# Kernel optimization log

Measured on AMD Instinct MI355X. Metric: run time of the kernel, lower is better.

## Reference

```python
import jax, jax.numpy as jnp
import numpy as np

N_USERS = 100000
N_ITEMS = 50000
N_NODES = N_USERS + N_ITEMS
N_EDGES = 3000000
EMBED_DIM = 64
N_LAYERS = 3


def setup_inputs() -> dict:
    key = jax.random.key(0)
    k1, k2, k3, k4, k5 = jax.random.split(key, 5)
    user_emb = 0.1 * jax.random.normal(k1, (N_USERS, EMBED_DIM), dtype=jnp.float32)
    item_emb = 0.1 * jax.random.normal(k2, (N_ITEMS, EMBED_DIM), dtype=jnp.float32)
    adj_rows = jax.random.randint(k3, (N_EDGES,), 0, N_NODES, dtype=jnp.int32)
    adj_cols = jax.random.randint(k4, (N_EDGES,), 0, N_NODES, dtype=jnp.int32)
    # mimic symmetric normalization scale (~1/avg_degree) so repeated SpMM stays stable
    avg_degree = N_EDGES / N_NODES
    adj_vals = jax.random.uniform(k5, (N_EDGES,), dtype=jnp.float32) / jnp.float32(avg_degree)
    return {"user_emb": user_emb, "item_emb": item_emb,
            "adj_rows": adj_rows, "adj_cols": adj_cols, "adj_vals": adj_vals}


def _spmm(rows, cols, vals, x):
    # y[r] = sum_{e: rows[e]==r} vals[e] * x[cols[e]]   (COO SpMM)
    msgs = vals[:, None] * x[cols]          # [E, d] gathered messages
    return jax.ops.segment_sum(msgs, rows, num_segments=N_NODES)


def reference(user_emb, item_emb, adj_rows, adj_cols, adj_vals):
    all_emb = jnp.concatenate([user_emb, item_emb], axis=0)  # [N, d]
    acc = all_emb
    cur = all_emb
    for _ in range(N_LAYERS):
        cur = _spmm(adj_rows, adj_cols, adj_vals, cur)
        acc = acc + cur
    final_emb = acc / jnp.float32(N_LAYERS + 1)  # mean over stacked layers
    return final_emb[:N_USERS], final_emb[N_USERS:]
```

## Files before the change

kernel.cpp:

```cpp
#include <hip/hip_runtime.h>
#include <cstddef>
#include <cstdint>

#define N_USERS 100000
#define N_ITEMS 50000
#define N_NODES 150000
#define N_EDGES 3000000

#define NBKT 586
#define BCHUNK 8192
#define ABLK ((N_EDGES + BCHUNK - 1) / BCHUNK)
#define NCLS 16
#define SCHUNK 3
#define PADMAX (256 * 7)

#define VMAX  0.05f
#define QSCALE (16384.0f / VMAX)
#define DEQ    (VMAX / 16384.0f)

typedef unsigned int uint32;
typedef unsigned short ushort16;

__device__ __forceinline__ ushort16 f2b(float f) {
    uint32 b = __float_as_uint(f);
    b += 0x7FFFu + ((b >> 16) & 1u);
    return (ushort16)(b >> 16);
}
__device__ __forceinline__ float b2f(ushort16 h) {
    return __uint_as_float(((uint32)h) << 16);
}

#define CVT_BLOCKS ((N_NODES * 16 + 255) / 256)

__global__ __launch_bounds__(256) void k_cvt_count(const float* __restrict__ user,
                                                   const float* __restrict__ item,
                                                   ushort16* __restrict__ allb,
                                                   const int* __restrict__ rows,
                                                   int* __restrict__ bucket_cnt) {
    if (blockIdx.x < CVT_BLOCKS) {
        int i = blockIdx.x * blockDim.x + threadIdx.x;
        const int total4 = N_NODES * 16;
        if (i >= total4) return;
        const int user4 = N_USERS * 16;
        float4 v = (i < user4) ? ((const float4*)user)[i]
                               : ((const float4*)item)[i - user4];
        ushort4 h;
        h.x = f2b(v.x); h.y = f2b(v.y); h.z = f2b(v.z); h.w = f2b(v.w);
        ((ushort4*)allb)[i] = h;
        return;
    }
    __shared__ int hist[NBKT];
    int t = threadIdx.x;
    for (int j = t; j < NBKT; j += 256) hist[j] = 0;
    __syncthreads();
    int blk = blockIdx.x - CVT_BLOCKS;
    int s0 = blk * BCHUNK;
    int e0 = min(s0 + BCHUNK, N_EDGES);
    for (int i = s0 + t * 4; i < e0; i += 1024) {
        int4 r4 = *(const int4*)(rows + i);
        atomicAdd(&hist[r4.x >> 8], 1); atomicAdd(&hist[r4.y >> 8], 1);
        atomicAdd(&hist[r4.z >> 8], 1); atomicAdd(&hist[r4.w >> 8], 1);
    }
    __syncthreads();
    for (int j = t; j < NBKT; j += 256)
        if (hist[j]) atomicAdd(&bucket_cnt[j], hist[j]);
}

__global__ __launch_bounds__(1024) void k_bucket_scan(const int* __restrict__ bucket_cnt,
                                                      int* __restrict__ bucket_start,
                                                      int* __restrict__ bucket_cursor) {
    __shared__ int sh[1024];
    int t = threadIdx.x;
    sh[t] = (t < NBKT) ? bucket_cnt[t] : 0;
    __syncthreads();
    for (int off = 1; off < 1024; off <<= 1) {
        int add = (t >= off) ? sh[t - off] : 0;
        __syncthreads();
        sh[t] += add;
        __syncthreads();
    }
    if (t < NBKT) {
        int st = (t == 0) ? 0 : sh[t - 1];
        bucket_start[t] = st;
        bucket_cursor[t] = st;
    }
    if (t == 0) bucket_start[NBKT] = N_EDGES;
}

__global__ __launch_bounds__(256) void k_bucket_scatter(const int* __restrict__ rows,
                                                        const int* __restrict__ cols,
                                                        const float* __restrict__ vals,
                                                        int* __restrict__ bucket_cursor,
                                                        int2* __restrict__ ebuf) {
    __shared__ int  hist[NBKT];
    __shared__ int  lstart[NBKT];
    __shared__ int  curs[NBKT];
    __shared__ int  gbase[NBKT];
    __shared__ int  psum[256];
    __shared__ int2 stage[BCHUNK];
    int t = threadIdx.x;
    for (int j = t; j < NBKT; j += 256) hist[j] = 0;
    __syncthreads();
    int s0 = blockIdx.x * BCHUNK;
    int e0 = min(s0 + BCHUNK, N_EDGES);
    int n = e0 - s0;
    for (int i = s0 + t * 4; i < e0; i += 1024) {
        int4 r4 = *(const int4*)(rows + i);
        atomicAdd(&hist[r4.x >> 8], 1); atomicAdd(&hist[r4.y >> 8], 1);
        atomicAdd(&hist[r4.z >> 8], 1); atomicAdd(&hist[r4.w >> 8], 1);
    }
    __syncthreads();
    int base = t * SCHUNK;
    int v0 = (base < NBKT) ? hist[base] : 0;
    int v1 = (base + 1 < NBKT) ? hist[base + 1] : 0;
    int v2 = (base + 2 < NBKT) ? hist[base + 2] : 0;
    psum[t] = v0 + v1 + v2;
    __syncthreads();
    for (int off = 1; off < 256; off <<= 1) {
        int add = (t >= off) ? psum[t - off] : 0;
        __syncthreads();
        psum[t] += add;
        __syncthreads();
    }
    int run = (t == 0) ? 0 : psum[t - 1];
    if (base < NBKT) {
        lstart[base] = run; curs[base] = run;
        if (v0) gbase[base] = atomicAdd(&bucket_cursor[base], v0);
        run += v0;
    }
    if (base + 1 < NBKT) {
        lstart[base + 1] = run; curs[base + 1] = run;
        if (v1) gbase[base + 1] = atomicAdd(&bucket_cursor[base + 1], v1);
        run += v1;
    }
    if (base + 2 < NBKT) {
        lstart[base + 2] = run; curs[base + 2] = run;
        if (v2) gbase[base + 2] = atomicAdd(&bucket_cursor[base + 2], v2);
        run += v2;
    }
    __syncthreads();
    for (int i = s0 + t * 4; i < e0; i += 1024) {
        int4   r4 = *(const int4*)(rows + i);
        int4   c4 = *(const int4*)(cols + i);
        float4 w4 = *(const float4*)(vals + i);
        int rr, cc, b, pos; float ww;
        rr = r4.x; cc = c4.x; ww = w4.x; b = rr >> 8;
        pos = atomicAdd(&curs[b], 1);
        stage[pos] = make_int2(cc | ((rr & 255) << 18), __float_as_int(ww));
        rr = r4.y; cc = c4.y; ww = w4.y; b = rr >> 8;
        pos = atomicAdd(&curs[b], 1);
        stage[pos] = make_int2(cc | ((rr & 255) << 18), __float_as_int(ww));
        rr = r4.z; cc = c4.z; ww = w4.z; b = rr >> 8;
        pos = atomicAdd(&curs[b], 1);
        stage[pos] = make_int2(cc | ((rr & 255) << 18), __float_as_int(ww));
        rr = r4.w; cc = c4.w; ww = w4.w; b = rr >> 8;
        pos = atomicAdd(&curs[b], 1);
        stage[pos] = make_int2(cc | ((rr & 255) << 18), __float_as_int(ww));
    }
    __syncthreads();
    for (int i = t; i < n; i += 256) {
        int2 ed = stage[i];
        int lo = 0, hi = NBKT - 1;
        while (lo < hi) {
            int mid = (lo + hi + 1) >> 1;
            if (lstart[mid] <= i) lo = mid; else hi = mid - 1;
        }
        int dst = gbase[lo] + (i - lstart[lo]);
        long long q; __builtin_memcpy(&q, &ed, 8);
        __builtin_nontemporal_store(q, (long long*)(ebuf + dst));
    }
}

__global__ __launch_bounds__(256) void k_csr_build(const int2* __restrict__ ebuf,
                                                   const int* __restrict__ bucket_start,
                                                   int* __restrict__ row_start,
                                                   int* __restrict__ row_end,
                                                   uint32* __restrict__ ecsr) {
    __shared__ int cnt2[256 * NCLS];
    __shared__ int psum[256];
    int b = blockIdx.x, t = threadIdx.x;
    int rbase = b << 8;
    for (int j = t; j < 256 * NCLS; j += 256) cnt2[j] = 0;
    __syncthreads();
    int s = bucket_start[b], e = bucket_start[b + 1];
    int wbase = s + b * PADMAX;
    for (int i = s + t; i < e; i += 256) {
        int2 ed = ebuf[i];
        int col = ed.x & 0x3FFFF;
        int key = (((ed.x >> 18) & 255) << 4) | (col >> 14);
        atomicAdd(&cnt2[key], 1);
    }
    __syncthreads();
    int base = t * NCLS;
    int vals[NCLS];
    int cnt_row = 0;
    #pragma unroll
    for (int j = 0; j < NCLS; ++j) { vals[j] = cnt2[base + j]; cnt_row += vals[j]; }
    int pcnt = (cnt_row + 7) & ~7;
    psum[t] = pcnt;
    __syncthreads();
    for (int off = 1; off < 256; off <<= 1) {
        int add = (t >= off) ? psum[t - off] : 0;
        __syncthreads();
        psum[t] += add;
        __syncthreads();
    }
    int run = psum[t] - pcnt;
    int rr = rbase + t;
    if (rr < N_NODES) {
        row_start[rr] = wbase + run;
        row_end[rr]   = wbase + run + pcnt;
    }
    int rl = run;
    #pragma unroll
    for (int j = 0; j < NCLS; ++j) { int c = vals[j]; cnt2[base + j] = rl; rl += c; }
    __syncthreads();
    for (int i = s + t; i < e; i += 256) {
        int2 ed = ebuf[i];
        int col = ed.x & 0x3FFFF;
        int key = (((ed.x >> 18) & 255) << 4) | (col >> 14);
        int pos = atomicAdd(&cnt2[key], 1);
        float w = __int_as_float(ed.y);
        int q = (int)(w * QSCALE + 0.5f);
        q = min(q, 16383);
        ecsr[wbase + pos] = (uint32)col | ((uint32)q << 18);
    }
    for (int j = cnt_row; j < pcnt; ++j) ecsr[wbase + run + j] = 0;
}

template <int LAYER>
__global__ __launch_bounds__(256) void k_spmm(const int* __restrict__ row_start,
                                              const int* __restrict__ row_end,
                                              const uint32* __restrict__ ecsr,
                                              const ushort16* __restrict__ x,
                                              ushort16* __restrict__ yb,
                                              const ushort16* __restrict__ e0b,
                                              const ushort16* __restrict__ y1b,
                                              float* __restrict__ out) {
    int gid = blockIdx.x * blockDim.x + threadIdx.x;
    int r = gid >> 6;
    int lane = threadIdx.x & 63;
    if (r >= N_NODES) return;
    int s = __builtin_amdgcn_readfirstlane(row_start[r]);
    int e = __builtin_amdgcn_readfirstlane(row_end[r]);
    float acc = 0.f;
    if (e > s) {
        uint32 c0 = __builtin_nontemporal_load(ecsr + s);
        uint32 c1 = __builtin_nontemporal_load(ecsr + s + 1);
        uint32 c2 = __builtin_nontemporal_load(ecsr + s + 2);
        uint32 c3 = __builtin_nontemporal_load(ecsr + s + 3);
        uint32 c4 = __builtin_nontemporal_load(ecsr + s + 4);
        uint32 c5 = __builtin_nontemporal_load(ecsr + s + 5);
        uint32 c6 = __builtin_nontemporal_load(ecsr + s + 6);
        uint32 c7 = __builtin_nontemporal_load(ecsr + s + 7);
        for (int i = s + 8; i < e; i += 8) {
            uint32 n0 = __builtin_nontemporal_load(ecsr + i);
            uint32 n1 = __builtin_nontemporal_load(ecsr + i + 1);
            uint32 n2 = __builtin_nontemporal_load(ecsr + i + 2);
            uint32 n3 = __builtin_nontemporal_load(ecsr + i + 3);
            uint32 n4 = __builtin_nontemporal_load(ecsr + i + 4);
            uint32 n5 = __builtin_nontemporal_load(ecsr + i + 5);
            uint32 n6 = __builtin_nontemporal_load(ecsr + i + 6);
            uint32 n7 = __builtin_nontemporal_load(ecsr + i + 7);
            acc += (float)(c0 >> 18) * b2f(x[(size_t)(c0 & 0x3FFFF) * 64 + lane]);
            acc += (float)(c1 >> 18) * b2f(x[(size_t)(c1 & 0x3FFFF) * 64 + lane]);
            acc += (float)(c2 >> 18) * b2f(x[(size_t)(c2 & 0x3FFFF) * 64 + lane]);
            acc += (float)(c3 >> 18) * b2f(x[(size_t)(c3 & 0x3FFFF) * 64 + lane]);
            acc += (float)(c4 >> 18) * b2f(x[(size_t)(c4 & 0x3FFFF) * 64 + lane]);
            acc += (float)(c5 >> 18) * b2f(x[(size_t)(c5 & 0x3FFFF) * 64 + lane]);
            acc += (float)(c6 >> 18) * b2f(x[(size_t)(c6 & 0x3FFFF) * 64 + lane]);
            acc += (float)(c7 >> 18) * b2f(x[(size_t)(c7 & 0x3FFFF) * 64 + lane]);
            c0 = n0; c1 = n1; c2 = n2; c3 = n3;
            c4 = n4; c5 = n5; c6 = n6; c7 = n7;
        }
        acc += (float)(c0 >> 18) * b2f(x[(size_t)(c0 & 0x3FFFF) * 64 + lane]);
        acc += (float)(c1 >> 18) * b2f(x[(size_t)(c1 & 0x3FFFF) * 64 + lane]);
        acc += (float)(c2 >> 18) * b2f(x[(size_t)(c2 & 0x3FFFF) * 64 + lane]);
        acc += (float)(c3 >> 18) * b2f(x[(size_t)(c3 & 0x3FFFF) * 64 + lane]);
        acc += (float)(c4 >> 18) * b2f(x[(size_t)(c4 & 0x3FFFF) * 64 + lane]);
        acc += (float)(c5 >> 18) * b2f(x[(size_t)(c5 & 0x3FFFF) * 64 + lane]);
        acc += (float)(c6 >> 18) * b2f(x[(size_t)(c6 & 0x3FFFF) * 64 + lane]);
        acc += (float)(c7 >> 18) * b2f(x[(size_t)(c7 & 0x3FFFF) * 64 + lane]);
        acc *= DEQ;
    }

    size_t o = (size_t)r * 64 + lane;
    if constexpr (LAYER == 3) {
        ushort16 h0 = __builtin_nontemporal_load((const unsigned short*)e0b + o);
        ushort16 h1 = __builtin_nontemporal_load((const unsigned short*)y1b + o);
        ushort16 h2 = __builtin_nontemporal_load((const unsigned short*)x + o);
        __builtin_nontemporal_store(0.25f * (b2f(h0) + b2f(h1) + b2f(h2) + acc), out + o);
    } else {
        __builtin_nontemporal_store(f2b(acc), (unsigned short*)yb + o);
    }
}

__global__ __launch_bounds__(256) void k_init(const float* __restrict__ user,
                                              const float* __restrict__ item,
                                              float* __restrict__ cur,
                                              float* __restrict__ out) {
    int i = blockIdx.x * blockDim.x + threadIdx.x;
    const int total4 = N_NODES * 16;
    if (i >= total4) return;
    const int user4 = N_USERS * 16;
    float4 v = (i < user4) ? ((const float4*)user)[i]
                           : ((const float4*)item)[i - user4];
    ((float4*)cur)[i] = v;
    ((float4*)out)[i] = make_float4(0.25f * v.x, 0.25f * v.y,
                                    0.25f * v.z, 0.25f * v.w);
}

__global__ __launch_bounds__(256) void k_edge_atomic(const int* __restrict__ rows,
                                                     const int* __restrict__ cols,
                                                     const float* __restrict__ vals,
                                                     const float* __restrict__ x,
                                                     float* __restrict__ y) {
    long long gid = (long long)blockIdx.x * blockDim.x + threadIdx.x;
    int e = (int)(gid >> 6);
    int lane = threadIdx.x & 63;
    if (e >= N_EDGES) return;
    int r = rows[e], c = cols[e];
    float v = vals[e];
    atomicAdd(&y[r * 64 + lane], v * x[c * 64 + lane]);
}

__global__ __launch_bounds__(256) void k_accum(const float* __restrict__ y,
                                               float* __restrict__ out) {
    int i = blockIdx.x * blockDim.x + threadIdx.x;
    const int total4 = N_NODES * 16;
    if (i >= total4) return;
    float4 a = ((const float4*)y)[i];
    float4 o = ((float4*)out)[i];
    o.x += 0.25f * a.x; o.y += 0.25f * a.y;
    o.z += 0.25f * a.z; o.w += 0.25f * a.w;
    ((float4*)out)[i] = o;
}

extern "C" void kernel_launch(void* const* d_in, const int* in_sizes, int n_in,
                              void* d_out, int out_size, void* d_ws, size_t ws_size,
                              hipStream_t stream) {
    const float* user = (const float*)d_in[0];
    const float* item = (const float*)d_in[1];
    const int*   rows = (const int*)d_in[2];
    const int*   cols = (const int*)d_in[3];
    const float* vals = (const float*)d_in[4];
    float* out = (float*)d_out;

    const int SPMM_BLOCKS = (N_NODES * 64 + 255) / 256;

    auto align256 = [](size_t x) { return (x + 255) & ~(size_t)255; };
    const size_t sz_embf = align256((size_t)N_NODES * 64 * sizeof(float));
    const size_t sz_embb = align256((size_t)N_NODES * 64 * sizeof(short));
    const size_t n_ecsr  = (size_t)N_EDGES + (size_t)NBKT * PADMAX;
    const size_t sz_ecsr = align256(n_ecsr * sizeof(uint32));
    const size_t sz_rs   = align256((size_t)(N_NODES + 1) * sizeof(int));
    const size_t sz_bk   = align256((size_t)(NBKT + 1) * sizeof(int));
    const size_t need_csr = 3 * sz_embb + sz_ecsr + 2 * sz_rs + 3 * sz_bk;

    char* p = (char*)d_ws;
    if (ws_size >= need_csr) {
        ushort16* allb = (ushort16*)p; p += sz_embb;
        ushort16* y1b  = (ushort16*)p; p += sz_embb;
        ushort16* y2b  = (ushort16*)p; p += sz_embb;
        uint32* ecsr     = (uint32*)p; p += sz_ecsr;
        int*   row_start = (int*)p;   p += sz_rs;
        int*   row_end   = (int*)p;   p += sz_rs;
        int*   bucket_cnt    = (int*)p; p += sz_bk;
        int*   bucket_start  = (int*)p; p += sz_bk;
        int*   bucket_cursor = (int*)p; p += sz_bk;
        int2*  ebuf = (int2*)y1b;

        hipMemsetAsync(bucket_cnt, 0, (size_t)NBKT * sizeof(int), stream);
        k_cvt_count<<<CVT_BLOCKS + ABLK, 256, 0, stream>>>(user, item, allb, rows, bucket_cnt);
        k_bucket_scan<<<1, 1024, 0, stream>>>(bucket_cnt, bucket_start, bucket_cursor);
        k_bucket_scatter<<<ABLK, 256, 0, stream>>>(rows, cols, vals, bucket_cursor, ebuf);
        k_csr_build<<<NBKT, 256, 0, stream>>>(ebuf, bucket_start, row_start, row_end, ecsr);

        k_spmm<1><<<SPMM_BLOCKS, 256, 0, stream>>>(row_start, row_end, ecsr, allb,
                                                   y1b, nullptr, nullptr, out);
        k_spmm<2><<<SPMM_BLOCKS, 256, 0, stream>>>(row_start, row_end, ecsr, y1b,
                                                   y2b, nullptr, nullptr, out);
        k_spmm<3><<<SPMM_BLOCKS, 256, 0, stream>>>(row_start, row_end, ecsr, y2b,
                                                   nullptr, allb, y1b, out);
    } else {
        float* bufA = (float*)p; p += sz_embf;
        float* bufB = (float*)p; p += sz_embf;
        float* in   = bufA;
        float* y    = bufB;
        const long long EA_THREADS = (long long)N_EDGES * 64;
        const int EA_BLOCKS = (int)((EA_THREADS + 255) / 256);

        k_init<<<CVT_BLOCKS, 256, 0, stream>>>(user, item, in, out);
        for (int l = 0; l < 3; ++l) {
            hipMemsetAsync(y, 0, (size_t)N_NODES * 64 * sizeof(float), stream);
            k_edge_atomic<<<EA_BLOCKS, 256, 0, stream>>>(rows, cols, vals, in, y);
            k_accum<<<CVT_BLOCKS, 256, 0, stream>>>(y, out);
            float* t = in; in = y; y = t;
        }
    }
}
```

Baseline: 309.5 us.

## Split wavefront into half-waves gathering packed bf16 pairs per edge

The SpMM kernel now has each 32-lane half of a wavefront load two bf16 features as one 32-bit word. Each half processes alternate edges of a group of eight, and the two halves are combined with a cross-lane shuffle at the end. The edge loop is also restructured into a two-stage software pipeline that issues the next group's index and feature gathers before accumulating the current group. This aims to halve the number of gather instructions per edge and put more loads in flight. In exchange the code is more complex, uses more registers, and half the lanes sit idle during the store.

Measured after the change: 289.1 us. 6.6% less time.

```diff
diff --git a/kernel.cpp b/kernel.cpp
--- a/kernel.cpp
+++ b/kernel.cpp
@@ -228,14 +228,44 @@
     for (int j = cnt_row; j < pcnt; ++j) ecsr[wbase + run + j] = 0;
 }
 
+#define LGRP(II, E0,E1,E2,E3, G0,G1,G2,G3) do { \
+    uint32 w0 = __builtin_nontemporal_load(ecsr + (II)); \
+    uint32 w1 = __builtin_nontemporal_load(ecsr + (II) + 1); \
+    uint32 w2 = __builtin_nontemporal_load(ecsr + (II) + 2); \
+    uint32 w3 = __builtin_nontemporal_load(ecsr + (II) + 3); \
+    uint32 w4 = __builtin_nontemporal_load(ecsr + (II) + 4); \
+    uint32 w5 = __builtin_nontemporal_load(ecsr + (II) + 5); \
+    uint32 w6 = __builtin_nontemporal_load(ecsr + (II) + 6); \
+    uint32 w7 = __builtin_nontemporal_load(ecsr + (II) + 7); \
+    E0 = half ? w1 : w0; E1 = half ? w3 : w2; \
+    E2 = half ? w5 : w4; E3 = half ? w7 : w6; \
+    G0 = xp[(size_t)(E0 & 0x3FFFF) * 32 + k]; \
+    G1 = xp[(size_t)(E1 & 0x3FFFF) * 32 + k]; \
+    G2 = xp[(size_t)(E2 & 0x3FFFF) * 32 + k]; \
+    G3 = xp[(size_t)(E3 & 0x3FFFF) * 32 + k]; \
+} while (0)
+
+#define AGRP(E0,E1,E2,E3, G0,G1,G2,G3) do { \
+    float q0 = (float)(E0 >> 18), q1 = (float)(E1 >> 18); \
+    float q2 = (float)(E2 >> 18), q3 = (float)(E3 >> 18); \
+    ax0 += q0 * __uint_as_float(G0 << 16); \
+    ay0 += q0 * __uint_as_float(G0 & 0xFFFF0000u); \
+    ax1 += q1 * __uint_as_float(G1 << 16); \
+    ay1 += q1 * __uint_as_float(G1 & 0xFFFF0000u); \
+    ax0 += q2 * __uint_as_float(G2 << 16); \
+    ay0 += q2 * __uint_as_float(G2 & 0xFFFF0000u); \
+    ax1 += q3 * __uint_as_float(G3 << 16); \
+    ay1 += q3 * __uint_as_float(G3 & 0xFFFF0000u); \
+} while (0)
+
 template <int LAYER>
 __global__ __launch_bounds__(256) void k_spmm(const int* __restrict__ row_start,
                                               const int* __restrict__ row_end,
                                               const uint32* __restrict__ ecsr,
-                                              const ushort16* __restrict__ x,
-                                              ushort16* __restrict__ yb,
-                                              const ushort16* __restrict__ e0b,
-                                              const ushort16* __restrict__ y1b,
+                                              const uint32* __restrict__ xp,
+                                              uint32* __restrict__ ybp,
+                                              const uint32* __restrict__ e0p,
+                                              const uint32* __restrict__ y1p,
                                               float* __restrict__ out) {
     int gid = blockIdx.x * blockDim.x + threadIdx.x;
     int r = gid >> 6;
@@ -243,55 +273,63 @@
     if (r >= N_NODES) return;
     int s = __builtin_amdgcn_readfirstlane(row_start[r]);
     int e = __builtin_amdgcn_readfirstlane(row_end[r]);
-    float acc = 0.f;
+    int half = lane >> 5;
+    int k = lane & 31;
+    float ax0 = 0.f, ay0 = 0.f, ax1 = 0.f, ay1 = 0.f;
+
     if (e > s) {
-        uint32 c0 = __builtin_nontemporal_load(ecsr + s);
-        uint32 c1 = __builtin_nontemporal_load(ecsr + s + 1);
-        uint32 c2 = __builtin_nontemporal_load(ecsr + s + 2);
-        uint32 c3 = __builtin_nontemporal_load(ecsr + s + 3);
-        uint32 c4 = __builtin_nontemporal_load(ecsr + s + 4);
-        uint32 c5 = __builtin_nontemporal_load(ecsr + s + 5);
-        uint32 c6 = __builtin_nontemporal_load(ecsr + s + 6);
-        uint32 c7 = __builtin_nontemporal_load(ecsr + s + 7);
-        for (int i = s + 8; i < e; i += 8) {
-            uint32 n0 = __builtin_nontemporal_load(ecsr + i);
-            uint32 n1 = __builtin_nontemporal_load(ecsr + i + 1);
-            uint32 n2 = __builtin_nontemporal_load(ecsr + i + 2);
-            uint32 n3 = __builtin_nontemporal_load(ecsr + i + 3);
-            uint32 n4 = __builtin_nontemporal_load(ecsr + i + 4);
-            uint32 n5 = __builtin_nontemporal_load(ecsr + i + 5);
-            uint32 n6 = __builtin_nontemporal_load(ecsr + i + 6);
-            uint32 n7 = __builtin_nontemporal_load(ecsr + i + 7);
-            acc += (float)(c0 >> 18) * b2f(x[(size_t)(c0 & 0x3FFFF) * 64 + lane]);
-            acc += (float)(c1 >> 18) * b2f(x[(size_t)(c1 & 0x3FFFF) * 64 + lane]);
-            acc += (float)(c2 >> 18) * b2f(x[(size_t)(c2 & 0x3FFFF) * 64 + lane]);
-            acc += (float)(c3 >> 18) * b2f(x[(size_t)(c3 & 0x3FFFF) * 64 + lane]);
-            acc += (float)(c4 >> 18) * b2f(x[(size_t)(c4 & 0x3FFFF) * 64 + lane]);
-            acc += (float)(c5 >> 18) * b2f(x[(size_t)(c5 & 0x3FFFF) * 64 + lane]);
-            acc += (float)(c6 >> 18) * b2f(x[(size_t)(c6 & 0x3FFFF) * 64 + lane]);
-            acc += (float)(c7 >> 18) * b2f(x[(size_t)(c7 & 0x3FFFF) * 64 + lane]);
-            c0 = n0; c1 = n1; c2 = n2; c3 = n3;
-            c4 = n4; c5 = n5; c6 = n6; c7 = n7;
+        uint32 A0, A1, A2, A3, GA0, GA1, GA2, GA3;
+        LGRP(s, A0,A1,A2,A3, GA0,GA1,GA2,GA3);
+        int ng = (e - s) >> 3;
+        if (ng > 1) {
+            uint32 B0, B1, B2, B3, GB0, GB1, GB2, GB3;
+            LGRP(s + 8, B0,B1,B2,B3, GB0,GB1,GB2,GB3);
+            int i = s + 16;
+            int rem = ng - 2;
+            while (rem >= 2) {
+                AGRP(A0,A1,A2,A3, GA0,GA1,GA2,GA3);
+                LGRP(i, A0,A1,A2,A3, GA0,GA1,GA2,GA3);
+                AGRP(B0,B1,B2,B3, GB0,GB1,GB2,GB3);
+                LGRP(i + 8, B0,B1,B2,B3, GB0,GB1,GB2,GB3);
+                i += 16; rem -= 2;
+            }
+            if (rem) {
+                AGRP(A0,A1,A2,A3, GA0,GA1,GA2,GA3);
+                LGRP(i, A0,A1,A2,A3, GA0,GA1,GA2,GA3);
+                AGRP(B0,B1,B2,B3, GB0,GB1,GB2,GB3);
+                AGRP(A0,A1,A2,A3, GA0,GA1,GA2,GA3);
+            } else {
+                AGRP(A0,A1,A2,A3, GA0,GA1,GA2,GA3);
+                AGRP(B0,B1,B2,B3, GB0,GB1,GB2,GB3);
+            }
+        } else {
+            AGRP(A0,A1,A2,A3, GA0,GA1,GA2,GA3);
         }
-        acc += (float)(c0 >> 18) * b2f(x[(size_t)(c0 & 0x3FFFF) * 64 + lane]);
-        acc += (float)(c1 >> 18) * b2f(x[(size_t)(c1 & 0x3FFFF) * 64 + lane]);
-        acc += (float)(c2 >> 18) * b2f(x[(size_t)(c2 & 0x3FFFF) * 64 + lane]);
-        acc += (float)(c3 >> 18) * b2f(x[(size_t)(c3 & 0x3FFFF) * 64 + lane]);
-        acc += (float)(c4 >> 18) * b2f(x[(size_t)(c4 & 0x3FFFF) * 64 + lane]);
-        acc += (float)(c5 >> 18) * b2f(x[(size_t)(c5 & 0x3FFFF) * 64 + lane]);
-        acc += (float)(c6 >> 18) * b2f(x[(size_t)(c6 & 0x3FFFF) * 64 + lane]);
-        acc += (float)(c7 >> 18) * b2f(x[(size_t)(c7 & 0x3FFFF) * 64 + lane]);
-        acc *= DEQ;
-    }
-
-    size_t o = (size_t)r * 64 + lane;
-    if constexpr (LAYER == 3) {
-        ushort16 h0 = __builtin_nontemporal_load((const unsigned short*)e0b + o);
-        ushort16 h1 = __builtin_nontemporal_load((const unsigned short*)y1b + o);
-        ushort16 h2 = __builtin_nontemporal_load((const unsigned short*)x + o);
-        __builtin_nontemporal_store(0.25f * (b2f(h0) + b2f(h1) + b2f(h2) + acc), out + o);
-    } else {
-        __builtin_nontemporal_store(f2b(acc), (unsigned short*)yb + o);
+    }
+
+    float ax = ax0 + ax1;
+    float ay = ay0 + ay1;
+    ax += __shfl_xor(ax, 32);
+    ay += __shfl_xor(ay, 32);
+    ax *= DEQ; ay *= DEQ;
+
+    if (half == 0) {
+        size_t op = (size_t)r * 32 + k;
+        if constexpr (LAYER == 3) {
+            uint32 h0 = __builtin_nontemporal_load(e0p + op);
+            uint32 h1 = __builtin_nontemporal_load(y1p + op);
+            uint32 h2 = xp[op];
+            float ox = 0.25f * (__uint_as_float(h0 << 16) + __uint_as_float(h1 << 16)
+                              + __uint_as_float(h2 << 16) + ax);
+            float oy = 0.25f * (__uint_as_float(h0 & 0xFFFF0000u)
+                              + __uint_as_float(h1 & 0xFFFF0000u)
+                              + __uint_as_float(h2 & 0xFFFF0000u) + ay);
+            __builtin_nontemporal_store(ox, out + 2 * op);
+            __builtin_nontemporal_store(oy, out + 2 * op + 1);
+        } else {
+            uint32 pk = (uint32)f2b(ax) | ((uint32)f2b(ay) << 16);
+            __builtin_nontemporal_store(pk, ybp + op);
+        }
     }
 }
 
@@ -376,12 +414,15 @@
         k_bucket_scatter<<<ABLK, 256, 0, stream>>>(rows, cols, vals, bucket_cursor, ebuf);
         k_csr_build<<<NBKT, 256, 0, stream>>>(ebuf, bucket_start, row_start, row_end, ecsr);
 
-        k_spmm<1><<<SPMM_BLOCKS, 256, 0, stream>>>(row_start, row_end, ecsr, allb,
-                                                   y1b, nullptr, nullptr, out);
-        k_spmm<2><<<SPMM_BLOCKS, 256, 0, stream>>>(row_start, row_end, ecsr, y1b,
-                                                   y2b, nullptr, nullptr, out);
-        k_spmm<3><<<SPMM_BLOCKS, 256, 0, stream>>>(row_start, row_end, ecsr, y2b,
-                                                   nullptr, allb, y1b, out);
+        k_spmm<1><<<SPMM_BLOCKS, 256, 0, stream>>>(row_start, row_end, ecsr,
+                                                   (const uint32*)allb, (uint32*)y1b,
+                                                   nullptr, nullptr, out);
+        k_spmm<2><<<SPMM_BLOCKS, 256, 0, stream>>>(row_start, row_end, ecsr,
+                                                   (const uint32*)y1b, (uint32*)y2b,
+                                                   nullptr, nullptr, out);
+        k_spmm<3><<<SPMM_BLOCKS, 256, 0, stream>>>(row_start, row_end, ecsr,
+                                                   (const uint32*)y2b, nullptr,
+                                                   (const uint32*)allb, (const uint32*)y1b, out);
     } else {
         float* bufA = (float*)p; p += sz_embf;
         float* bufB = (float*)p; p += sz_embf;
```
